# Kernel optimization log

Hardware: AMD Instinct MI355X
Metric: run time of the kernel (lower is better)

## Reference

```python
import jax, jax.numpy as jnp
import numpy as np

B, L, D, H, I = 4, 2048, 768, 12, 3072
HD = D // H  # 64
EPS = 1e-5


def _ln(x, g, b):
    mu = jnp.mean(x, axis=-1, keepdims=True)
    var = jnp.var(x, axis=-1, keepdims=True)
    return (x - mu) * jax.lax.rsqrt(var + EPS) * g + b


def setup_inputs() -> dict:
    key = jax.random.key(0)
    ks = jax.random.split(key, 8)
    s = 0.02
    return {
        "x": jax.random.normal(ks[0], (B, L, D), dtype=jnp.float32),
        "attention_mask": jnp.ones((B, L), dtype=bool),
        "ln1_g": jnp.ones((D,), jnp.float32),
        "ln1_b": jnp.zeros((D,), jnp.float32),
        "w_qkv": jax.random.normal(ks[1], (D, 3 * D), jnp.float32) * s,
        "b_qkv": jnp.zeros((3 * D,), jnp.float32),
        "w_o": jax.random.normal(ks[2], (D, D), jnp.float32) * s,
        "b_o": jnp.zeros((D,), jnp.float32),
        "ln2_g": jnp.ones((D,), jnp.float32),
        "ln2_b": jnp.zeros((D,), jnp.float32),
        "w1": jax.random.normal(ks[3], (D, I), jnp.float32) * s,
        "b1": jnp.zeros((I,), jnp.float32),
        "w2": jax.random.normal(ks[4], (I, D), jnp.float32) * s,
        "b2": jnp.zeros((D,), jnp.float32),
    }


def reference(x, attention_mask, ln1_g, ln1_b, w_qkv, b_qkv, w_o, b_o,
              ln2_g, ln2_b, w1, b1, w2, b2):
    # pre-LN + fused qkv projection
    h = _ln(x, ln1_g, ln1_b)
    qkv = h @ w_qkv + b_qkv                      # [B,L,3D]
    qkv = qkv.reshape(B, L, H, 3 * HD)           # chunk per-head: first HD=q, then k, then v
    q, k, v = qkv[..., :HD], qkv[..., HD:2 * HD], qkv[..., 2 * HD:]
    # NOTE: original divides by head_dim (q.size(-1)), NOT sqrt(head_dim)
    scores = jnp.einsum('blhd,bmhd->bhlm', q, k) / HD   # [B,H,L,L]
    causal = jnp.tril(jnp.ones((L, L), dtype=bool))
    full_mask = attention_mask[:, None, None, :] & causal
    scores = jnp.where(full_mask, scores, -jnp.inf)
    p = jax.nn.softmax(scores, axis=-1)
    attn = jnp.einsum('bhlm,bmhd->blhd', p, v).reshape(B, L, D)
    out_attn = attn @ w_o + b_o + x
    # FFN: Sequential(Linear, Linear, GELU, Dropout) -> GELU applied LAST (faithful to source)
    h2 = _ln(out_attn, ln2_g, ln2_b)
    ff = jax.nn.gelu((h2 @ w1 + b1) @ w2 + b2, approximate=False)
    return out_attn + ff
```

## Files before the change

### kernel.cpp

```cpp
#include <hip/hip_runtime.h>
#include <stdint.h>

typedef __attribute__((ext_vector_type(8))) short short8;
typedef __attribute__((ext_vector_type(4))) float f32x4;

typedef const void __attribute__((address_space(1)))* gas1_t;
typedef void __attribute__((address_space(3)))* las3_t;
#define GLL16(g, l) __builtin_amdgcn_global_load_lds((gas1_t)(const void*)(g), (las3_t)(void*)(l), 16, 0, 0)

__device__ __forceinline__ unsigned short f2bf(float x){
  union { float f; unsigned u; } c; c.f = x;
  return (unsigned short)((c.u + 0x7fffu + ((c.u >> 16) & 1u)) >> 16);
}

__device__ __forceinline__ short8 pack_bf16x8(f32x4 a, f32x4 b){
  union { unsigned u[4]; short8 s8; } r;
  asm("v_cvt_pk_bf16_f32 %0, %1, %2" : "=v"(r.u[0]) : "v"(a[0]), "v"(a[1]));
  asm("v_cvt_pk_bf16_f32 %0, %1, %2" : "=v"(r.u[1]) : "v"(a[2]), "v"(a[3]));
  asm("v_cvt_pk_bf16_f32 %0, %1, %2" : "=v"(r.u[2]) : "v"(b[0]), "v"(b[1]));
  asm("v_cvt_pk_bf16_f32 %0, %1, %2" : "=v"(r.u[3]) : "v"(b[2]), "v"(b[3]));
  return r.s8;
}

constexpr int Bc = 4, Lc = 2048, Dc = 768, Hc = 12, HDc = 64, Ic = 3072;
constexpr int Mrows = Bc * Lc;
constexpr int N3 = 3 * Dc;

__global__ void transpose_w(const float* __restrict__ W, unsigned short* __restrict__ Wt, int K, int N){
  __shared__ float t[32][33];
  int n0 = blockIdx.x * 32, k0 = blockIdx.y * 32;
  int tx = threadIdx.x, ty = threadIdx.y;
  #pragma unroll
  for (int j = 0; j < 4; ++j)
    t[ty + 8*j][tx] = W[(size_t)(k0 + ty + 8*j) * N + n0 + tx];
  __syncthreads();
  #pragma unroll
  for (int j = 0; j < 4; ++j)
    Wt[(size_t)(n0 + ty + 8*j) * K + k0 + tx] = f2bf(t[tx][ty + 8*j]);
}

__global__ void transpose_v(const unsigned short* __restrict__ qkv, unsigned short* __restrict__ vt){
  __shared__ unsigned short t[32][33];
  int l0 = blockIdx.x * 32, d0 = blockIdx.y * 32;
  int bh = blockIdx.z; int b = bh / Hc, h = bh - b * Hc;
  int tx = threadIdx.x, ty = threadIdx.y;
  const unsigned short* src = qkv + (size_t)b * Lc * N3 + h * 192 + 128;
  #pragma unroll
  for (int j = 0; j < 4; ++j)
    t[ty + 8*j][tx] = src[(size_t)(l0 + ty + 8*j) * N3 + d0 + tx];
  __syncthreads();
  unsigned short* dst = vt + (size_t)bh * 64 * Lc;
  #pragma unroll
  for (int j = 0; j < 4; ++j)
    dst[(size_t)(d0 + ty + 8*j) * Lc + l0 + tx] = t[tx][ty + 8*j];
}

__global__ __launch_bounds__(256) void ln_kernel(const float* __restrict__ x, const float* __restrict__ g,
                                                 const float* __restrict__ bta, unsigned short* __restrict__ out){
  int row = blockIdx.x, tid = threadIdx.x;
  const float* xr = x + (size_t)row * 768;
  float v0 = xr[tid], v1 = xr[tid + 256], v2 = xr[tid + 512];
  float s = v0 + v1 + v2;
  float ss = v0*v0 + v1*v1 + v2*v2;
  #pragma unroll
  for (int o = 32; o > 0; o >>= 1){ s += __shfl_xor(s, o); ss += __shfl_xor(ss, o); }
  __shared__ float red[8];
  int w = tid >> 6;
  if ((tid & 63) == 0){ red[w] = s; red[4 + w] = ss; }
  __syncthreads();
  s  = red[0] + red[1] + red[2] + red[3];
  ss = red[4] + red[5] + red[6] + red[7];
  float mu  = s * (1.f / 768.f);
  float var = ss * (1.f / 768.f) - mu * mu;
  float rs  = rsqrtf(var + 1e-5f);
  unsigned short* orow = out + (size_t)row * 768;
  orow[tid]       = f2bf((v0 - mu) * rs * g[tid]       + bta[tid]);
  orow[tid + 256] = f2bf((v1 - mu) * rs * g[tid + 256] + bta[tid + 256]);
  orow[tid + 512] = f2bf((v2 - mu) * rs * g[tid + 512] + bta[tid + 512]);
}

template<int MODE>
__global__ __launch_bounds__(512, 1) void gemm_bt(
    const unsigned short* __restrict__ A, const unsigned short* __restrict__ Bt,
    const float* __restrict__ bias, const float* __restrict__ res,
    void* __restrict__ outp, int Kdim, int Ndim)
{
  __shared__ __align__(16) unsigned short Als[2][128 * 64];
  __shared__ __align__(16) unsigned short Bls[2][128 * 64];
  int tid = threadIdx.x, w = tid >> 6, lane = tid & 63;
  int g = lane >> 4, r16 = lane & 15;
  int wm = w >> 2, wn = w & 3;

  int nwg = gridDim.x * gridDim.y;
  int flat = blockIdx.y * gridDim.x + blockIdx.x;
  int cpx = nwg >> 3;
  int swz = (flat & 7) * cpx + (flat >> 3);
  int bx = swz % gridDim.x, by = swz / gridDim.x;
  int m0 = by * 128, n0 = bx * 128;

  f32x4 acc[4][2];
  #pragma unroll
  for (int m = 0; m < 4; ++m)
    #pragma unroll
    for (int n = 0; n < 2; ++n) acc[m][n] = f32x4{0.f, 0.f, 0.f, 0.f};

  int lrow = lane >> 3;
  int gsw8 = ((lane & 7) ^ lrow) * 8;
  auto stage = [&](int buf, int kt){
    int k0 = kt * 64;
    #pragma unroll
    for (int i = 0; i < 2; ++i){
      int c = w * 2 + i;
      int row = c * 8 + lrow;
      GLL16(A  + (size_t)(m0 + row) * Kdim + k0 + gsw8, &Als[buf][c * 512]);
      GLL16(Bt + (size_t)(n0 + row) * Kdim + k0 + gsw8, &Bls[buf][c * 512]);
    }
  };

  int nk = Kdim >> 6;
  stage(0, 0);
  int cur = 0;
  for (int kt = 0; kt < nk; ++kt){
    __builtin_amdgcn_s_barrier();
    if (kt + 1 < nk){
      stage(cur ^ 1, kt + 1);
      asm volatile("s_waitcnt vmcnt(4)" ::: "memory");
    } else {
      asm volatile("s_waitcnt vmcnt(0)" ::: "memory");
    }
    __builtin_amdgcn_s_barrier();

    #pragma unroll
    for (int ks = 0; ks < 2; ++ks){
      short8 af[4], bfv[2];
      #pragma unroll
      for (int m = 0; m < 4; ++m){
        int r = wm * 64 + m * 16 + r16;
        af[m] = *(const short8*)&Als[cur][r * 64 + (((ks*4 + g) ^ (r & 7)) << 3)];
      }
      #pragma unroll
      for (int n = 0; n < 2; ++n){
        int r = wn * 32 + n * 16 + r16;
        bfv[n] = *(const short8*)&Bls[cur][r * 64 + (((ks*4 + g) ^ (r & 7)) << 3)];
      }
      #pragma unroll
      for (int m = 0; m < 4; ++m)
        #pragma unroll
        for (int n = 0; n < 2; ++n)
          acc[m][n] = __builtin_amdgcn_mfma_f32_16x16x32_bf16(af[m], bfv[n], acc[m][n], 0, 0, 0);
    }
    cur ^= 1;
  }

  #pragma unroll
  for (int n = 0; n < 2; ++n){
    int col = n0 + wn * 32 + n * 16 + r16;
    float bv = bias[col];
    #pragma unroll
    for (int m = 0; m < 4; ++m){
      #pragma unroll
      for (int j = 0; j < 4; ++j){
        int rowg = m0 + wm * 64 + m * 16 + g * 4 + j;
        size_t idx = (size_t)rowg * Ndim + col;
        float v = acc[m][n][j] + bv;
        if (MODE == 0){
          ((unsigned short*)outp)[idx] = f2bf(v);
        } else if (MODE == 1){
          ((float*)outp)[idx] = v + res[idx];
        } else {
          float ge = 0.5f * v * (1.0f + erff(v * 0.70710678118f));
          ((float*)outp)[idx] = res[idx] + ge;
        }
      }
    }
  }
}

__global__ __launch_bounds__(256, 2) void attn_kernel(const unsigned short* __restrict__ qkv,
                                                      const unsigned short* __restrict__ vt,
                                                      unsigned short* __restrict__ attn_out){
  int qt = 31 - blockIdx.y;
  int bh = blockIdx.x;
  int b = bh / Hc, h = bh - b * Hc;
  int tid = threadIdx.x, w = tid >> 6, lane = tid & 63;
  int g = lane >> 4, r16 = lane & 15;
  const unsigned short* base  = qkv + (size_t)b * Lc * N3 + h * 192;
  const unsigned short* vbase = vt + (size_t)bh * 64 * Lc;

  __shared__ __align__(16) unsigned short Kls[2][64 * 64];
  __shared__ __align__(16) unsigned short Vls[2][64 * 64];
  __shared__ __align__(16) float Pls[4][16 * 64];

  int qw = qt * 64 + w * 16;
  short8 qf[2];
  #pragma unroll
  for (int dh = 0; dh < 2; ++dh)
    qf[dh] = *(const short8*)(base + (size_t)(qw + r16) * N3 + dh*32 + g*8);

  f32x4 o[4];
  #pragma unroll
  for (int nd = 0; nd < 4; ++nd) o[nd] = f32x4{0.f, 0.f, 0.f, 0.f};
  float l_part[4] = {0.f, 0.f, 0.f, 0.f};

  float* Pw = &Pls[w][0];
  constexpr float SM_SCALE = 0.022542110013890052f;

  int lrow = lane >> 3, csw8 = ((lane & 7) ^ lrow) * 8;
  auto stage = [&](int buf, int kt){
    #pragma unroll
    for (int i = 0; i < 2; ++i){
      int r0 = (w * 2 + i) * 8;
      int row = r0 + lrow;
      GLL16(base  + (size_t)(kt*64 + row) * N3 + 64 + csw8, &Kls[buf][r0 * 64]);
      GLL16(vbase + (size_t)row * Lc + kt*64 + csw8,        &Vls[buf][r0 * 64]);
    }
  };

  auto compute_tile = [&](int cur, int kt, bool diag){
    f32x4 s[4];
    #pragma unroll
    for (int nk = 0; nk < 4; ++nk) s[nk] = f32x4{0.f,0.f,0.f,0.f};
    #pragma unroll
    for (int nk = 0; nk < 4; ++nk){
      int krow = nk*16 + r16;
      #pragma unroll
      for (int dh = 0; dh < 2; ++dh){
        short8 kf = *(const short8*)&Kls[cur][krow * 64 + (((dh*4 + g) ^ (krow & 7)) << 3)];
        s[nk] = __builtin_amdgcn_mfma_f32_16x16x32_bf16(qf[dh], kf, s[nk], 0, 0, 0);
      }
    }
    int qv = qw + g*4;
    #pragma unroll
    for (int nk = 0; nk < 4; ++nk){
      int kc = kt*64 + nk*16 + r16;
      #pragma unroll
      for (int j = 0; j < 4; ++j){
        float t = s[nk][j] * SM_SCALE;
        if (diag) t = (kc <= qv + j) ? t : -1e30f;
        float p = __builtin_amdgcn_exp2f(t);
        l_part[j] += p;
        int row = g*4 + j, col = nk*16 + r16;
        Pw[(row << 6) + ((((col >> 2) ^ (row & 7)) << 2) | (col & 3))] = p;
      }
    }
    asm volatile("" ::: "memory");
    #pragma unroll
    for (int ks = 0; ks < 2; ++ks){
      int gr0 = (ks*8 + g*2) ^ (r16 & 7);
      int gr1 = (ks*8 + g*2 + 1) ^ (r16 & 7);
      f32x4 pa = *(const f32x4*)&Pw[(r16 << 6) + (gr0 << 2)];
      f32x4 pb = *(const f32x4*)&Pw[(r16 << 6) + (gr1 << 2)];
      short8 pf = pack_bf16x8(pa, pb);
      #pragma unroll
      for (int nd = 0; nd < 4; ++nd){
        int vrow = nd*16 + r16;
        short8 vf = *(const short8*)&Vls[cur][vrow * 64 + (((ks*4 + g) ^ (vrow & 7)) << 3)];
        o[nd] = __builtin_amdgcn_mfma_f32_16x16x32_bf16(pf, vf, o[nd], 0, 0, 0);
      }
    }
  };

  stage(0, 0);
  __syncthreads();
  int cur = 0;
  for (int kt = 0; kt < qt; ++kt){
    stage(cur ^ 1, kt + 1);
    compute_tile(cur, kt, false);
    __syncthreads();
    cur ^= 1;
  }
  compute_tile(cur, qt, true);

  #pragma unroll
  for (int off = 8; off > 0; off >>= 1)
    #pragma unroll
    for (int j = 0; j < 4; ++j) l_part[j] += __shfl_xor(l_part[j], off);
  float inv[4];
  #pragma unroll
  for (int j = 0; j < 4; ++j) inv[j] = 1.0f / l_part[j];

  unsigned short* ob = attn_out + (size_t)b * Lc * Dc + h * HDc;
  #pragma unroll
  for (int nd = 0; nd < 4; ++nd)
    #pragma unroll
    for (int j = 0; j < 4; ++j){
      int q2 = qw + g*4 + j;
      ob[(size_t)q2 * Dc + nd*16 + r16] = f2bf(o[nd][j] * inv[j]);
    }
}

extern "C" void kernel_launch(void* const* d_in, const int* in_sizes, int n_in,
                              void* d_out, int out_size, void* d_ws, size_t ws_size,
                              hipStream_t stream){
  const float* x     = (const float*)d_in[0];
  const float* ln1_g = (const float*)d_in[2];
  const float* ln1_b = (const float*)d_in[3];
  const float* w_qkv = (const float*)d_in[4];
  const float* b_qkv = (const float*)d_in[5];
  const float* w_o   = (const float*)d_in[6];
  const float* b_o   = (const float*)d_in[7];
  const float* ln2_g = (const float*)d_in[8];
  const float* ln2_b = (const float*)d_in[9];
  const float* w1    = (const float*)d_in[10];
  const float* b1    = (const float*)d_in[11];
  const float* w2    = (const float*)d_in[12];
  const float* b2    = (const float*)d_in[13];

  char* ws = (char*)d_ws;
  size_t off = 0;
  auto alloc = [&](size_t bytes){ void* p = ws + off; off += (bytes + 255) & ~(size_t)255; return p; };
  unsigned short* wqkv_t = (unsigned short*)alloc((size_t)N3 * Dc * 2);
  unsigned short* wo_t   = (unsigned short*)alloc((size_t)Dc * Dc * 2);
  unsigned short* w1_t   = (unsigned short*)alloc((size_t)Ic * Dc * 2);
  unsigned short* w2_t   = (unsigned short*)alloc((size_t)Dc * Ic * 2);
  unsigned short* hbuf   = (unsigned short*)alloc((size_t)Mrows * Dc * 2);
  float*          oattn  = (float*)alloc((size_t)Mrows * Dc * 4);
  unsigned short* vtb    = (unsigned short*)alloc((size_t)Bc * Hc * HDc * Lc * 2);
  char*           big    = (char*)alloc((size_t)Mrows * Ic * 2);
  unsigned short* qkv    = (unsigned short*)big;
  unsigned short* attn_o = (unsigned short*)(big + (size_t)Mrows * N3 * 2);
  unsigned short* ff1    = (unsigned short*)big;

  dim3 tb(32, 8, 1);
  transpose_w<<<dim3(N3/32, Dc/32), tb, 0, stream>>>(w_qkv, wqkv_t, Dc, N3);
  transpose_w<<<dim3(Dc/32, Dc/32), tb, 0, stream>>>(w_o,   wo_t,   Dc, Dc);
  transpose_w<<<dim3(Ic/32, Dc/32), tb, 0, stream>>>(w1,    w1_t,   Dc, Ic);
  transpose_w<<<dim3(Dc/32, Ic/32), tb, 0, stream>>>(w2,    w2_t,   Ic, Dc);

  ln_kernel<<<dim3(Mrows), dim3(256), 0, stream>>>(x, ln1_g, ln1_b, hbuf);

  gemm_bt<0><<<dim3(N3/128, Mrows/128), dim3(512), 0, stream>>>(hbuf, wqkv_t, b_qkv, nullptr, (void*)qkv, Dc, N3);

  transpose_v<<<dim3(Lc/32, HDc/32, Bc*Hc), tb, 0, stream>>>(qkv, vtb);

  attn_kernel<<<dim3(Bc*Hc, Lc/64), dim3(256), 0, stream>>>(qkv, vtb, attn_o);

  gemm_bt<1><<<dim3(Dc/128, Mrows/128), dim3(512), 0, stream>>>(attn_o, wo_t, b_o, x, (void*)oattn, Dc, Dc);

  ln_kernel<<<dim3(Mrows), dim3(256), 0, stream>>>(oattn, ln2_g, ln2_b, hbuf);

  gemm_bt<0><<<dim3(Ic/128, Mrows/128), dim3(512), 0, stream>>>(hbuf, w1_t, b1, nullptr, (void*)ff1, Dc, Ic);

  gemm_bt<2><<<dim3(Dc/128, Mrows/128), dim3(512), 0, stream>>>(ff1, w2_t, b2, oattn, d_out, Ic, Dc);
}
```

Before: 268.0 us.

## Add 128x256-tile GEMM kernel for QKV and FFN-up projections

Adds a gemm_wide kernel with a 128x256 output tile per 512-thread block. Each wave computes a 64x64 sub-tile as 4x4 MFMA 16x16x32 bf16 fragments. The B (weight) tile is double-buffered through global_load_lds, while the A tile is single-buffered and loaded each k-step. The QKV and W1 projections now use this kernel. The aim is more reuse of each A tile and fewer blocks re-reading activations; the cost is larger LDS use per block, lower occupancy, and A-load latency that is not hidden behind compute.

```diff
diff --git a/kernel.cpp b/kernel.cpp
--- a/kernel.cpp
+++ b/kernel.cpp
@@ -77,6 +77,114 @@
   orow[tid]       = f2bf((v0 - mu) * rs * g[tid]       + bta[tid]);
   orow[tid + 256] = f2bf((v1 - mu) * rs * g[tid + 256] + bta[tid + 256]);
   orow[tid + 512] = f2bf((v2 - mu) * rs * g[tid + 512] + bta[tid + 512]);
+}
+
+template<int MODE>
+__global__ __launch_bounds__(512, 4) void gemm_wide(
+    const unsigned short* __restrict__ A, const unsigned short* __restrict__ Bt,
+    const float* __restrict__ bias, const float* __restrict__ res,
+    void* __restrict__ outp, int Kdim, int Ndim)
+{
+  __shared__ __align__(16) unsigned short Als[128 * 64];
+  __shared__ __align__(16) unsigned short Bls[2][256 * 64];
+  int tid = threadIdx.x, w = tid >> 6, lane = tid & 63;
+  int g = lane >> 4, r16 = lane & 15;
+  int wm = w >> 2, wn = w & 3;
+
+  int nwg = gridDim.x * gridDim.y;
+  int flat = blockIdx.y * gridDim.x + blockIdx.x;
+  int cpx = nwg >> 3;
+  int swz = (flat & 7) * cpx + (flat >> 3);
+  int bx = swz % gridDim.x, by = swz / gridDim.x;
+  int m0 = by * 128, n0 = bx * 256;
+
+  f32x4 acc[4][4];
+  #pragma unroll
+  for (int m = 0; m < 4; ++m)
+    #pragma unroll
+    for (int n = 0; n < 4; ++n) acc[m][n] = f32x4{0.f, 0.f, 0.f, 0.f};
+
+  int lrow = lane >> 3;
+  int gsw8 = ((lane & 7) ^ lrow) * 8;
+  auto stageA = [&](int kt){
+    int k0 = kt * 64;
+    #pragma unroll
+    for (int i = 0; i < 2; ++i){
+      int c = w * 2 + i;
+      int row = c * 8 + lrow;
+      GLL16(A + (size_t)(m0 + row) * Kdim + k0 + gsw8, &Als[c * 512]);
+    }
+  };
+  auto stageB = [&](int buf, int kt){
+    int k0 = kt * 64;
+    #pragma unroll
+    for (int i = 0; i < 4; ++i){
+      int c = w * 4 + i;
+      int row = c * 8 + lrow;
+      GLL16(Bt + (size_t)(n0 + row) * Kdim + k0 + gsw8, &Bls[buf][c * 512]);
+    }
+  };
+
+  int nk = Kdim >> 6;
+  stageB(0, 0);
+  int cur = 0;
+  for (int kt = 0; kt < nk; ++kt){
+    __builtin_amdgcn_s_barrier();
+    stageA(kt);
+    if (kt + 1 < nk){
+      stageB(cur ^ 1, kt + 1);
+      asm volatile("s_waitcnt vmcnt(4)" ::: "memory");
+    } else {
+      asm volatile("s_waitcnt vmcnt(0)" ::: "memory");
+    }
+    __builtin_amdgcn_s_barrier();
+
+    #pragma unroll
+    for (int ks = 0; ks < 2; ++ks){
+      short8 af[4], bfv[4];
+      #pragma unroll
+      for (int m = 0; m < 4; ++m){
+        int r = wm * 64 + m * 16 + r16;
+        af[m] = *(const short8*)&Als[r * 64 + (((ks*4 + g) ^ (r & 7)) << 3)];
+      }
+      #pragma unroll
+      for (int n = 0; n < 4; ++n){
+        int r = wn * 64 + n * 16 + r16;
+        bfv[n] = *(const short8*)&Bls[cur][r * 64 + (((ks*4 + g) ^ (r & 7)) << 3)];
+      }
+      __builtin_amdgcn_s_setprio(1);
+      #pragma unroll
+      for (int m = 0; m < 4; ++m)
+        #pragma unroll
+        for (int n = 0; n < 4; ++n)
+          acc[m][n] = __builtin_amdgcn_mfma_f32_16x16x32_bf16(af[m], bfv[n], acc[m][n], 0, 0, 0);
+      __builtin_amdgcn_s_setprio(0);
+    }
+    cur ^= 1;
+  }
+
+  #pragma unroll
+  for (int n = 0; n < 4; ++n){
+    int col = n0 + wn * 64 + n * 16 + r16;
+    float bv = bias[col];
+    #pragma unroll
+    for (int m = 0; m < 4; ++m){
+      #pragma unroll
+      for (int j = 0; j < 4; ++j){
+        int rowg = m0 + wm * 64 + m * 16 + g * 4 + j;
+        size_t idx = (size_t)rowg * Ndim + col;
+        float v = acc[m][n][j] + bv;
+        if (MODE == 0){
+          ((unsigned short*)outp)[idx] = f2bf(v);
+        } else if (MODE == 1){
+          ((float*)outp)[idx] = v + res[idx];
+        } else {
+          float ge = 0.5f * v * (1.0f + erff(v * 0.70710678118f));
+          ((float*)outp)[idx] = res[idx] + ge;
+        }
+      }
+    }
+  }
 }
 
 template<int MODE>
@@ -329,7 +437,7 @@
 
   ln_kernel<<<dim3(Mrows), dim3(256), 0, stream>>>(x, ln1_g, ln1_b, hbuf);
 
-  gemm_bt<0><<<dim3(N3/128, Mrows/128), dim3(512), 0, stream>>>(hbuf, wqkv_t, b_qkv, nullptr, (void*)qkv, Dc, N3);
+  gemm_wide<0><<<dim3(N3/256, Mrows/128), dim3(512), 0, stream>>>(hbuf, wqkv_t, b_qkv, nullptr, (void*)qkv, Dc, N3);
 
   transpose_v<<<dim3(Lc/32, HDc/32, Bc*Hc), tb, 0, stream>>>(qkv, vtb);
 
@@ -339,7 +447,7 @@
 
   ln_kernel<<<dim3(Mrows), dim3(256), 0, stream>>>(oattn, ln2_g, ln2_b, hbuf);
 
-  gemm_bt<0><<<dim3(Ic/128, Mrows/128), dim3(512), 0, stream>>>(hbuf, w1_t, b1, nullptr, (void*)ff1, Dc, Ic);
+  gemm_wide<0><<<dim3(Ic/256, Mrows/128), dim3(512), 0, stream>>>(hbuf, w1_t, b1, nullptr, (void*)ff1, Dc, Ic);
 
   gemm_bt<2><<<dim3(Dc/128, Mrows/128), dim3(512), 0, stream>>>(ff1, w2_t, b2, oattn, d_out, Ic, Dc);
 }
```

Measured after the change: 261.7 us. -2.4%, faster.
